# Kernel optimization log

Measured on AMD Instinct MI355X. Metric: run time of the kernel, lower is better.

The kernel has to match this reference:

```python
import jax, jax.numpy as jnp
import numpy as np

WIN = (2, 7, 7)
SHIFT = (1, 3, 3)
HEADS = 4
DIM = 128
MLP_HID = 512
N = WIN[0] * WIN[1] * WIN[2]  # 98
EPS = 1e-5


def _rel_pos_index():
    d = np.arange(WIN[0]); h = np.arange(WIN[1]); w = np.arange(WIN[2])
    coords = np.stack(np.meshgrid(d, h, w, indexing='ij'))  # (3, Wd, Wh, Ww)
    flat = coords.reshape(3, -1)  # (3, N)
    rel = flat[:, :, None] - flat[:, None, :]  # (3, N, N)
    rel = rel.transpose(1, 2, 0).astype(np.int64)  # (N, N, 3)
    rel[..., 0] += WIN[0] - 1
    rel[..., 1] += WIN[1] - 1
    rel[..., 2] += WIN[2] - 1
    rel[..., 0] *= (2 * WIN[1] - 1) * (2 * WIN[2] - 1)
    rel[..., 1] *= (2 * WIN[2] - 1)
    return rel.sum(-1)  # (N, N)


def setup_inputs() -> dict:
    key = jax.random.key(0)
    ks = jax.random.split(key, 8)
    B, D, H, W, C = 4, 8, 56, 56, DIM
    tbl_size = (2 * WIN[0] - 1) * (2 * WIN[1] - 1) * (2 * WIN[2] - 1)  # 507
    s = 0.02
    return {
        'x': jax.random.normal(ks[0], (B, D, H, W, C), jnp.float32),
        'rel_idx': jnp.asarray(_rel_pos_index(), jnp.int32),
        'rpb_table': s * jax.random.normal(ks[1], (tbl_size, HEADS), jnp.float32),
        'qkv_w': s * jax.random.normal(ks[2], (C, 3 * C), jnp.float32),
        'qkv_b': jnp.zeros((3 * C,), jnp.float32),
        'proj_w': s * jax.random.normal(ks[3], (C, C), jnp.float32),
        'proj_b': jnp.zeros((C,), jnp.float32),
        'ln1_g': jnp.ones((C,), jnp.float32),
        'ln1_b': jnp.zeros((C,), jnp.float32),
        'ln2_g': jnp.ones((C,), jnp.float32),
        'ln2_b': jnp.zeros((C,), jnp.float32),
        'mlp_w1': s * jax.random.normal(ks[4], (C, MLP_HID), jnp.float32),
        'mlp_b1': jnp.zeros((MLP_HID,), jnp.float32),
        'mlp_w2': s * jax.random.normal(ks[5], (MLP_HID, C), jnp.float32),
        'mlp_b2': jnp.zeros((C,), jnp.float32),
    }


def _layernorm(x, g, b):
    mu = jnp.mean(x, -1, keepdims=True)
    var = jnp.var(x, -1, keepdims=True)
    return (x - mu) * jax.lax.rsqrt(var + EPS) * g + b


def _window_partition(x):
    B, Dp, Hp, Wp, C = x.shape
    x = x.reshape(B, Dp // WIN[0], WIN[0], Hp // WIN[1], WIN[1], Wp // WIN[2], WIN[2], C)
    x = x.transpose(0, 1, 3, 5, 2, 4, 6, 7)
    return x.reshape(-1, N, C)


def _window_reverse(win, B, Dp, Hp, Wp):
    C = win.shape[-1]
    x = win.reshape(B, Dp // WIN[0], Hp // WIN[1], Wp // WIN[2], WIN[0], WIN[1], WIN[2], C)
    x = x.transpose(0, 1, 4, 2, 5, 3, 6, 7)
    return x.reshape(B, Dp, Hp, Wp, C)


def _block(x, rel_idx, rpb_table, qkv_w, qkv_b, proj_w, proj_b,
           ln1_g, ln1_b, ln2_g, ln2_b, mlp_w1, mlp_b1, mlp_w2, mlp_b2):
    B, D, H, W, C = x.shape
    shortcut = x
    x = _layernorm(x, ln1_g, ln1_b)
    pad_d = (-D) % WIN[0]; pad_h = (-H) % WIN[1]; pad_w = (-W) % WIN[2]
    x = jnp.pad(x, ((0, 0), (0, pad_d), (0, pad_h), (0, pad_w), (0, 0)))
    _, Dp, Hp, Wp, _ = x.shape
    x = jnp.roll(x, (-SHIFT[0], -SHIFT[1], -SHIFT[2]), axis=(1, 2, 3))
    xw = _window_partition(x)  # (B_, N, C)
    B_ = xw.shape[0]
    hd = C // HEADS
    qkv = (xw @ qkv_w + qkv_b).reshape(B_, N, 3, HEADS, hd).transpose(2, 0, 3, 1, 4)
    q, k, v = qkv[0], qkv[1], qkv[2]  # (B_, h, N, hd)
    q = q * (hd ** -0.5)
    attn = jnp.einsum('bhnd,bhmd->bhnm', q, k)
    bias = rpb_table[rel_idx.reshape(-1)].reshape(N, N, HEADS).transpose(2, 0, 1)
    attn = attn + bias[None]
    # NOTE: the original module calls attn with mask=None even when shifted.
    attn = jax.nn.softmax(attn, axis=-1)
    out = jnp.einsum('bhnm,bhmd->bhnd', attn, v).transpose(0, 2, 1, 3).reshape(B_, N, C)
    out = out @ proj_w + proj_b
    x = _window_reverse(out, B, Dp, Hp, Wp)
    x = jnp.roll(x, (SHIFT[0], SHIFT[1], SHIFT[2]), axis=(1, 2, 3))
    x = x[:, :D, :H, :W, :]
    x = shortcut + x
    h1 = _layernorm(x, ln2_g, ln2_b)
    h1 = jax.nn.gelu(h1 @ mlp_w1 + mlp_b1, approximate=False)
    return x + (h1 @ mlp_w2 + mlp_b2)


def reference(x, rel_idx, rpb_table, qkv_w, qkv_b, proj_w, proj_b,
              ln1_g, ln1_b, ln2_g, ln2_b, mlp_w1, mlp_b1, mlp_w2, mlp_b2):
    return _block(x, rel_idx, rpb_table, qkv_w, qkv_b, proj_w, proj_b,
                  ln1_g, ln1_b, ln2_g, ln2_b, mlp_w1, mlp_b1, mlp_w2, mlp_b2)
```

## Files before the change

kernel.cpp:

```cpp
#include <hip/hip_runtime.h>
#include <hip/hip_bf16.h>
#include <cstdint>

#define NWIN   1024
#define NTOK   98
#define BIAS_N 9604

typedef __attribute__((ext_vector_type(8))) short bf16x8;
typedef __attribute__((ext_vector_type(4))) float f32x4;

__device__ __forceinline__ float b2f(unsigned short u) {
  union { uint32_t i; float f; } v; v.i = ((uint32_t)u) << 16; return v.f;
}
__device__ __forceinline__ float b2f_lo(uint32_t u) {
  union { uint32_t i; float f; } v; v.i = u << 16; return v.f;
}
__device__ __forceinline__ float b2f_hi(uint32_t u) {
  union { uint32_t i; float f; } v; v.i = u & 0xffff0000u; return v.f;
}
__device__ __forceinline__ unsigned short f2b(float f) {
  union { float f; uint32_t i; } v; v.f = f;
  uint32_t r = v.i + 0x7fffu + ((v.i >> 16) & 1u);
  return (unsigned short)(r >> 16);
}
__device__ __forceinline__ float ldf(const void* p, size_t i, int f32) {
  return f32 ? ((const float*)p)[i] : b2f(((const unsigned short*)p)[i]);
}
__device__ __forceinline__ void stf(void* p, size_t i, int f32, float v) {
  if (f32) ((float*)p)[i] = v;
  else     ((unsigned short*)p)[i] = f2b(v);
}
__device__ __forceinline__ float2 ldf2(const void* p, size_t i, int f32) {
  if (f32) { const float* q = (const float*)p + i; return make_float2(q[0], q[1]); }
  uint32_t u = *(const uint32_t*)((const unsigned short*)p + i);
  return make_float2(b2f_lo(u), b2f_hi(u));
}

#define QG_OFF   0
#define KG_OFF   25690112
#define VG_OFF   51380224
#define BIAS_OFF 77070336
#define WQ_OFF   77224000
#define WP_OFF   77322304
#define W1_OFF   77355072
#define W2_OFF   77486144
#define PAR_OFF  77617216
#define FLAG_OFF 77623872
#define P_LN1G 0
#define P_LN1B 128
#define P_LN2G 256
#define P_LN2B 384
#define P_QKVB 512
#define P_PROJB 896
#define P_B1  1024
#define P_B2  1536

__global__ __launch_bounds__(256) void detect_kernel(const uint32_t* __restrict__ xw,
                                                     int* __restrict__ flag) {
  __shared__ int cnt;
  if (threadIdx.x == 0) cnt = 0;
  __syncthreads();
  uint32_t w = xw[threadIdx.x];
  int e = (w >> 23) & 0xFF;
  if (e >= 112 && e <= 134) atomicAdd(&cnt, 1);
  __syncthreads();
  if (threadIdx.x == 0) *flag = (cnt >= 128) ? 1 : 0;
}

__global__ __launch_bounds__(256) void prep_kernel(
    const void* __restrict__ qkvw, const void* __restrict__ projw,
    const void* __restrict__ w1, const void* __restrict__ w2,
    const void* __restrict__ ln1g, const void* __restrict__ ln1b,
    const void* __restrict__ ln2g, const void* __restrict__ ln2b,
    const void* __restrict__ qkvb, const void* __restrict__ projb,
    const void* __restrict__ b1, const void* __restrict__ b2,
    const int* __restrict__ flag,
    unsigned short* __restrict__ wq_t, unsigned short* __restrict__ wp_t,
    unsigned short* __restrict__ w1_t, unsigned short* __restrict__ w2_t,
    float* __restrict__ par) {
  const int f32 = *flag;
  int idx = blockIdx.x * 256 + threadIdx.x;
  if (idx < 49152) {
    int n = idx >> 7, k = idx & 127;
    wq_t[idx] = f2b(ldf(qkvw, (size_t)k * 384 + n, f32));
  } else if ((idx -= 49152) < 16384) {
    int n = idx >> 7, k = idx & 127;
    wp_t[idx] = f2b(ldf(projw, (size_t)k * 128 + n, f32));
  } else if ((idx -= 16384) < 65536) {
    int n = idx >> 7, k = idx & 127;
    w1_t[idx] = f2b(ldf(w1, (size_t)k * 512 + n, f32));
  } else if ((idx -= 65536) < 65536) {
    int n = idx >> 9, k = idx & 511;
    w2_t[idx] = f2b(ldf(w2, (size_t)k * 128 + n, f32));
  } else if ((idx -= 65536) < 1664) {
    float v;
    if      (idx < 128)  v = ldf(ln1g, idx, f32);
    else if (idx < 256)  v = ldf(ln1b, idx - 128, f32);
    else if (idx < 384)  v = ldf(ln2g, idx - 256, f32);
    else if (idx < 512)  v = ldf(ln2b, idx - 384, f32);
    else if (idx < 896)  v = ldf(qkvb, idx - 512, f32);
    else if (idx < 1024) v = ldf(projb, idx - 896, f32);
    else if (idx < 1536) v = ldf(b1, idx - 1024, f32);
    else                 v = ldf(b2, idx - 1536, f32);
    par[idx] = v;
  }
}

__global__ __launch_bounds__(256) void bias_kernel(const int* __restrict__ rel_idx,
                                                   const void* __restrict__ tbl,
                                                   const int* __restrict__ flag,
                                                   float* __restrict__ bias) {
  const int f32 = *flag;
  int i = blockIdx.x * 256 + threadIdx.x;
  if (i >= 4 * BIAS_N) return;
  int h = i / BIAS_N, ij = i % BIAS_N;
  bias[i] = ldf(tbl, (size_t)rel_idx[ij] * 4 + h, f32);
}

__global__ __launch_bounds__(256) void qkv_win_kernel(
    const void* __restrict__ x, const int* __restrict__ flag,
    const unsigned short* __restrict__ wq_t, const float* __restrict__ par,
    unsigned short* __restrict__ qg, unsigned short* __restrict__ kg,
    unsigned short* __restrict__ vg) {
  __shared__ unsigned short lnx[112 * 136];
  const int f32 = *flag;
  const int tid = threadIdx.x, wave = tid >> 6, lane = tid & 63;
  const int quad = lane >> 4, lcol = lane & 15;
  const int win = blockIdx.x;
  const int bb = win >> 8, r = win & 255;
  const int wd = r >> 6, r2 = r & 63, wh = r2 >> 3, ww = r2 & 7;

  for (int t = wave; t < NTOK; t += 4) {
    int td = t / 49, r3 = t % 49, th = r3 / 7, tw = r3 % 7;
    int sd = (wd * 2 + td + 1) & 7;
    int sh = (wh * 7 + th + 3) % 56;
    int sw = (ww * 7 + tw + 3) % 56;
    size_t src = ((((size_t)bb * 8 + sd) * 56 + sh) * 56 + sw) * 128;
    int c0 = lane * 2;
    float2 f = ldf2(x, src + c0, f32);
    float s = f.x + f.y, ss = f.x * f.x + f.y * f.y;
#pragma unroll
    for (int off = 32; off >= 1; off >>= 1) { s += __shfl_xor(s, off); ss += __shfl_xor(ss, off); }
    float mu = s * (1.0f / 128.0f);
    float var = ss * (1.0f / 128.0f) - mu * mu;
    float rs = rsqrtf(var + 1e-5f);
    float y0 = (f.x - mu) * rs * par[P_LN1G + c0] + par[P_LN1B + c0];
    float y1 = (f.y - mu) * rs * par[P_LN1G + c0 + 1] + par[P_LN1B + c0 + 1];
    *(uint32_t*)(lnx + t * 136 + c0) = (uint32_t)f2b(y0) | ((uint32_t)f2b(y1) << 16);
  }
  for (int i = tid; i < 14 * 68; i += 256) {
    int rr = i / 68, c = i % 68;
    *(uint32_t*)(lnx + (98 + rr) * 136 + c * 2) = 0u;
  }
  __syncthreads();

  for (int p = 0; p < 6; ++p) {
    const int n = p * 64 + wave * 16 + lcol;
    bf16x8 bfr[4];
#pragma unroll
    for (int ks = 0; ks < 4; ++ks)
      bfr[ks] = *(const bf16x8*)(wq_t + (size_t)n * 128 + ks * 32 + quad * 8);
    const int region = n >> 7, cc = n & 127, head = cc >> 5, d = cc & 31;
    unsigned short* dst = (region == 0 ? qg : (region == 1 ? kg : vg)) +
                          (((size_t)win * 4 + head) * NTOK) * 32 + d;
    const float bc = par[P_QKVB + n];
    const float scale = region == 0 ? 0.17677669529663687f : 1.0f;
    for (int mt = 0; mt < 7; ++mt) {
      f32x4 acc = (f32x4){0.f, 0.f, 0.f, 0.f};
#pragma unroll
      for (int ks = 0; ks < 4; ++ks) {
        bf16x8 a = *(const bf16x8*)(lnx + (mt * 16 + lcol) * 136 + ks * 32 + quad * 8);
        acc = __builtin_amdgcn_mfma_f32_16x16x32_bf16(a, bfr[ks], acc, 0, 0, 0);
      }
#pragma unroll
      for (int rr = 0; rr < 4; ++rr) {
        int m = mt * 16 + quad * 4 + rr;
        if (m < NTOK) dst[m * 32] = f2b((acc[rr] + bc) * scale);
      }
    }
  }
}

__global__ __launch_bounds__(256) void attn_fused_kernel(
    const unsigned short* __restrict__ qg, const unsigned short* __restrict__ kg,
    const unsigned short* __restrict__ vg, const float* __restrict__ bias,
    const unsigned short* __restrict__ wp_t, const float* __restrict__ par,
    const void* __restrict__ x, const int* __restrict__ flag,
    void* __restrict__ out) {
  __shared__ __align__(16) unsigned short smem[26112];
  const int f32 = *flag;
  const int tid = threadIdx.x, wave = tid >> 6, lane = tid & 63;
  const int quad = lane >> 4, lcol = lane & 15;
  const int win = blockIdx.x, h = wave;
  const size_t hb = (((size_t)win * 4 + h) * NTOK) * 32;

  unsigned short* vth = smem + h * (32 * 136);
  unsigned short* plh = smem + 17408 + h * (16 * 136);

  {
    const uint32_t* vsrc = (const uint32_t*)(vg + hb);
    for (int idx = lane; idx < NTOK * 16; idx += 64) {
      int j = idx >> 4, dp = idx & 15;
      uint32_t u = vsrc[idx];
      vth[(2 * dp) * 136 + j]     = (unsigned short)(u & 0xffffu);
      vth[(2 * dp + 1) * 136 + j] = (unsigned short)(u >> 16);
    }
    for (int idx = lane; idx < 32 * 30; idx += 64) {
      int d = idx / 30, c = 98 + idx % 30;
      vth[d * 136 + c] = 0;
    }
    for (int idx = lane; idx < 16 * 16; idx += 64) {
      int rr = idx >> 4, c = 112 + (idx & 15);
      plh[rr * 136 + c] = 0;
    }
  }

  bf16x8 aq[7], bk[7];
#pragma unroll
  for (int t = 0; t < 7; ++t) {
    int row = min(t * 16 + lcol, NTOK - 1);
    aq[t] = *(const bf16x8*)(qg + hb + (size_t)row * 32 + quad * 8);
    bk[t] = *(const bf16x8*)(kg + hb + (size_t)row * 32 + quad * 8);
  }

  const float* bh = bias + h * BIAS_N;
  f32x4 o[7][2];
  for (int mt = 0; mt < 7; ++mt) {
    f32x4 s[7];
#pragma unroll
    for (int nt = 0; nt < 7; ++nt)
      s[nt] = __builtin_amdgcn_mfma_f32_16x16x32_bf16(aq[mt], bk[nt],
                                                      (f32x4){0.f, 0.f, 0.f, 0.f}, 0, 0, 0);
    const int ib = mt * 16 + quad * 4;
#pragma unroll
    for (int nt = 0; nt < 7; ++nt) {
      int j = nt * 16 + lcol;
      bool jv = j < NTOK;
#pragma unroll
      for (int r = 0; r < 4; ++r) {
        int ic = min(ib + r, NTOK - 1);
        s[nt][r] = jv ? (s[nt][r] + bh[ic * NTOK + j]) : -3.0e38f;
      }
    }
    float mx[4], sum[4], inv[4];
#pragma unroll
    for (int r = 0; r < 4; ++r) {
      float m = s[0][r];
#pragma unroll
      for (int nt = 1; nt < 7; ++nt) m = fmaxf(m, s[nt][r]);
      mx[r] = m;
    }
#pragma unroll
    for (int off = 1; off < 16; off <<= 1)
#pragma unroll
      for (int r = 0; r < 4; ++r) mx[r] = fmaxf(mx[r], __shfl_xor(mx[r], off));
#pragma unroll
    for (int r = 0; r < 4; ++r) sum[r] = 0.f;
#pragma unroll
    for (int nt = 0; nt < 7; ++nt)
#pragma unroll
      for (int r = 0; r < 4; ++r) {
        float e = __expf(s[nt][r] - mx[r]);
        s[nt][r] = e; sum[r] += e;
      }
#pragma unroll
    for (int off = 1; off < 16; off <<= 1)
#pragma unroll
      for (int r = 0; r < 4; ++r) sum[r] += __shfl_xor(sum[r], off);
#pragma unroll
    for (int r = 0; r < 4; ++r) inv[r] = 1.0f / sum[r];
#pragma unroll
    for (int nt = 0; nt < 7; ++nt)
#pragma unroll
      for (int r = 0; r < 4; ++r)
        plh[(quad * 4 + r) * 136 + nt * 16 + lcol] = f2b(s[nt][r] * inv[r]);
#pragma unroll
    for (int n2 = 0; n2 < 2; ++n2) {
      f32x4 acc = (f32x4){0.f, 0.f, 0.f, 0.f};
#pragma unroll
      for (int kp = 0; kp < 4; ++kp) {
        bf16x8 a = *(const bf16x8*)(plh + lcol * 136 + kp * 32 + quad * 8);
        bf16x8 b = *(const bf16x8*)(vth + (n2 * 16 + lcol) * 136 + kp * 32 + quad * 8);
        acc = __builtin_amdgcn_mfma_f32_16x16x32_bf16(a, b, acc, 0, 0, 0);
      }
      o[mt][n2] = acc;
    }
  }
  __syncthreads();

  unsigned short* olds = smem;
#pragma unroll
  for (int mt = 0; mt < 7; ++mt)
#pragma unroll
    for (int n2 = 0; n2 < 2; ++n2)
#pragma unroll
      for (int r = 0; r < 4; ++r)
        olds[(mt * 16 + quad * 4 + r) * 136 + h * 32 + n2 * 16 + lcol] = f2b(o[mt][n2][r]);
  __syncthreads();

  f32x4 pr[2][7];
  for (int t2 = 0; t2 < 2; ++t2) {
    const int n = (h * 2 + t2) * 16 + lcol;
    bf16x8 bw[4];
#pragma unroll
    for (int kp = 0; kp < 4; ++kp)
      bw[kp] = *(const bf16x8*)(wp_t + (size_t)n * 128 + kp * 32 + quad * 8);
    for (int mt = 0; mt < 7; ++mt) {
      f32x4 acc = (f32x4){0.f, 0.f, 0.f, 0.f};
#pragma unroll
      for (int kp = 0; kp < 4; ++kp) {
        bf16x8 a = *(const bf16x8*)(olds + (mt * 16 + lcol) * 136 + kp * 32 + quad * 8);
        acc = __builtin_amdgcn_mfma_f32_16x16x32_bf16(a, bw[kp], acc, 0, 0, 0);
      }
      pr[t2][mt] = acc;
    }
  }
  __syncthreads();

  float* pout = (float*)smem;
  for (int t2 = 0; t2 < 2; ++t2) {
    const int n = (h * 2 + t2) * 16 + lcol;
    const float bc = par[P_PROJB + n];
#pragma unroll
    for (int mt = 0; mt < 7; ++mt)
#pragma unroll
      for (int r = 0; r < 4; ++r) {
        int m = mt * 16 + quad * 4 + r;
        if (m < NTOK) pout[m * 132 + n] = pr[t2][mt][r] + bc;
      }
  }
  __syncthreads();

  const int bb = win >> 8, rW = win & 255;
  const int wd = rW >> 6, r2 = rW & 63, wh = r2 >> 3, ww = r2 & 7;
  const int c = (tid & 31) * 4;
  for (int m = tid >> 5; m < NTOK; m += 8) {
    int td = m / 49, r3 = m % 49, th = r3 / 7, tw = r3 % 7;
    int sd = (wd * 2 + td + 1) & 7;
    int sh = (wh * 7 + th + 3) % 56;
    int sw = (ww * 7 + tw + 3) % 56;
    size_t base = ((((size_t)bb * 8 + sd) * 56 + sh) * 56 + sw) * 128 + c;
    float4 p = *(const float4*)(pout + m * 132 + c);
    if (f32) {
      const float4 xr = *(const float4*)((const float*)x + base);
      float4 ov = make_float4(p.x + xr.x, p.y + xr.y, p.z + xr.z, p.w + xr.w);
      *(float4*)((float*)out + base) = ov;
    } else {
      const ushort4 xr = *(const ushort4*)((const unsigned short*)x + base);
      ushort4 ov;
      ov.x = f2b(p.x + b2f(xr.x)); ov.y = f2b(p.y + b2f(xr.y));
      ov.z = f2b(p.z + b2f(xr.z)); ov.w = f2b(p.w + b2f(xr.w));
      *(ushort4*)((unsigned short*)out + base) = ov;
    }
  }
}

__global__ __launch_bounds__(256) void mlp_kernel(
    const unsigned short* __restrict__ w1_t, const unsigned short* __restrict__ w2_t,
    const float* __restrict__ par, const int* __restrict__ flag,
    void* __restrict__ out) {
  __shared__ __align__(16) unsigned short lnt[32 * 136];
  __shared__ __align__(16) unsigned short hbuf[32 * 264];
  const int f32 = *flag;
  const int tid = threadIdx.x, wave = tid >> 6, lane = tid & 63;
  const int quad = lane >> 4, lcol = lane & 15;
  const int m0 = blockIdx.x * 32;

  for (int t = wave; t < 32; t += 4) {
    int c0 = lane * 2;
    float2 f = ldf2(out, (size_t)(m0 + t) * 128 + c0, f32);
    float s = f.x + f.y, ss = f.x * f.x + f.y * f.y;
#pragma unroll
    for (int off = 32; off >= 1; off >>= 1) { s += __shfl_xor(s, off); ss += __shfl_xor(ss, off); }
    float mu = s * (1.0f / 128.0f);
    float var = ss * (1.0f / 128.0f) - mu * mu;
    float rs = rsqrtf(var + 1e-5f);
    float y0 = (f.x - mu) * rs * par[P_LN2G + c0] + par[P_LN2B + c0];
    float y1 = (f.y - mu) * rs * par[P_LN2G + c0 + 1] + par[P_LN2B + c0 + 1];
    *(uint32_t*)(lnt + t * 136 + c0) = (uint32_t)f2b(y0) | ((uint32_t)f2b(y1) << 16);
  }
  __syncthreads();

  f32x4 acc2[2][2];
#pragma unroll
  for (int a = 0; a < 2; ++a)
#pragma unroll
    for (int b = 0; b < 2; ++b) acc2[a][b] = (f32x4){0.f, 0.f, 0.f, 0.f};

  for (int g = 0; g < 2; ++g) {
    for (int p = 0; p < 4; ++p) {
      const int nl = p * 64 + wave * 16 + lcol;
      const int n = g * 256 + nl;
      bf16x8 bfr[4];
#pragma unroll
      for (int ks = 0; ks < 4; ++ks)
        bfr[ks] = *(const bf16x8*)(w1_t + (size_t)n * 128 + ks * 32 + quad * 8);
      const float bc = par[P_B1 + n];
#pragma unroll
      for (int mt = 0; mt < 2; ++mt) {
        f32x4 acc = (f32x4){0.f, 0.f, 0.f, 0.f};
#pragma unroll
        for (int ks = 0; ks < 4; ++ks) {
          bf16x8 a = *(const bf16x8*)(lnt + (mt * 16 + lcol) * 136 + ks * 32 + quad * 8);
          acc = __builtin_amdgcn_mfma_f32_16x16x32_bf16(a, bfr[ks], acc, 0, 0, 0);
        }
#pragma unroll
        for (int rr = 0; rr < 4; ++rr) {
          int m = mt * 16 + quad * 4 + rr;
          float v = acc[rr] + bc;
          v = 0.5f * v * (1.0f + erff(v * 0.70710678118654752f));
          hbuf[m * 264 + nl] = f2b(v);
        }
      }
    }
    __syncthreads();

#pragma unroll
    for (int np = 0; np < 2; ++np) {
      const int n = np * 64 + wave * 16 + lcol;
      for (int kp = 0; kp < 2; ++kp) {
        bf16x8 bfr[4];
#pragma unroll
        for (int ks = 0; ks < 4; ++ks)
          bfr[ks] = *(const bf16x8*)(w2_t + (size_t)n * 512 + g * 256 + kp * 128 +
                                     ks * 32 + quad * 8);
#pragma unroll
        for (int mt = 0; mt < 2; ++mt) {
#pragma unroll
          for (int ks = 0; ks < 4; ++ks) {
            bf16x8 a = *(const bf16x8*)(hbuf + (mt * 16 + lcol) * 264 + kp * 128 +
                                        ks * 32 + quad * 8);
            acc2[np][mt] = __builtin_amdgcn_mfma_f32_16x16x32_bf16(a, bfr[ks], acc2[np][mt], 0, 0, 0);
          }
        }
      }
    }
    __syncthreads();
  }

  float* pout = (float*)hbuf;
#pragma unroll
  for (int np = 0; np < 2; ++np) {
    const int n = np * 64 + wave * 16 + lcol;
    const float bc = par[P_B2 + n];
#pragma unroll
    for (int mt = 0; mt < 2; ++mt)
#pragma unroll
      for (int rr = 0; rr < 4; ++rr)
        pout[(mt * 16 + quad * 4 + rr) * 132 + n] = acc2[np][mt][rr] + bc;
  }
  __syncthreads();

  for (int i = tid; i < 1024; i += 256) {
    int t = i >> 5, c = (i & 31) * 4;
    size_t base = (size_t)(m0 + t) * 128 + c;
    float4 p = *(const float4*)(pout + t * 132 + c);
    if (f32) {
      const float4 xr = *(const float4*)((const float*)out + base);
      float4 ov = make_float4(p.x + xr.x, p.y + xr.y, p.z + xr.z, p.w + xr.w);
      *(float4*)((float*)out + base) = ov;
    } else {
      const ushort4 xr = *(const ushort4*)((const unsigned short*)out + base);
      ushort4 ov;
      ov.x = f2b(p.x + b2f(xr.x)); ov.y = f2b(p.y + b2f(xr.y));
      ov.z = f2b(p.z + b2f(xr.z)); ov.w = f2b(p.w + b2f(xr.w));
      *(ushort4*)((unsigned short*)out + base) = ov;
    }
  }
}

extern "C" void kernel_launch(void* const* d_in, const int* in_sizes, int n_in,
                              void* d_out, int out_size, void* d_ws, size_t ws_size,
                              hipStream_t stream) {
  const void* x      = d_in[0];
  const int*  rel    = (const int*)d_in[1];
  const void* rpb    = d_in[2];
  const void* qkv_w  = d_in[3];
  const void* qkv_b  = d_in[4];
  const void* proj_w = d_in[5];
  const void* proj_b = d_in[6];
  const void* ln1_g  = d_in[7];
  const void* ln1_b  = d_in[8];
  const void* ln2_g  = d_in[9];
  const void* ln2_b  = d_in[10];
  const void* w1     = d_in[11];
  const void* b1     = d_in[12];
  const void* w2     = d_in[13];
  const void* b2     = d_in[14];

  char* ws = (char*)d_ws;
  unsigned short* qg   = (unsigned short*)(ws + QG_OFF);
  unsigned short* kg   = (unsigned short*)(ws + KG_OFF);
  unsigned short* vg   = (unsigned short*)(ws + VG_OFF);
  float*          bias = (float*)(ws + BIAS_OFF);
  unsigned short* wq_t = (unsigned short*)(ws + WQ_OFF);
  unsigned short* wp_t = (unsigned short*)(ws + WP_OFF);
  unsigned short* w1_t = (unsigned short*)(ws + W1_OFF);
  unsigned short* w2_t = (unsigned short*)(ws + W2_OFF);
  float*          par  = (float*)(ws + PAR_OFF);
  int*            flag = (int*)(ws + FLAG_OFF);

  detect_kernel<<<1, 256, 0, stream>>>((const uint32_t*)x, flag);
  prep_kernel<<<775, 256, 0, stream>>>(qkv_w, proj_w, w1, w2, ln1_g, ln1_b, ln2_g,
                                       ln2_b, qkv_b, proj_b, b1, b2, flag,
                                       wq_t, wp_t, w1_t, w2_t, par);
  bias_kernel<<<(4 * BIAS_N + 255) / 256, 256, 0, stream>>>(rel, rpb, flag, bias);
  qkv_win_kernel<<<NWIN, 256, 0, stream>>>(x, flag, wq_t, par, qg, kg, vg);
  attn_fused_kernel<<<NWIN, 256, 0, stream>>>(qg, kg, vg, bias, wp_t, par, x, flag, d_out);
  mlp_kernel<<<100352 / 32, 256, 0, stream>>>(w1_t, w2_t, par, flag, d_out);
}
```

Before: 431.5 us.

## Write V pre-transposed from QKV kernel and shrink attention LDS footprint

The QKV projection kernel now writes V directly in a transposed, zero-padded (d x 112) layout to global memory, so the attention kernel reads V fragments straight from global instead of transposing V through shared memory. The attention kernel's LDS drops from about 52KB to about 30KB. The projection-output staging is split into two 56-row passes to fit the smaller buffer, and launch bounds now request 4 blocks per CU. The aim is higher occupancy and no per-block transpose, at the cost of an extra barrier pass and uncached global V loads inside the PV matmul.

```diff
diff --git a/kernel.cpp b/kernel.cpp
--- a/kernel.cpp
+++ b/kernel.cpp
@@ -38,14 +38,15 @@
 
 #define QG_OFF   0
 #define KG_OFF   25690112
-#define VG_OFF   51380224
-#define BIAS_OFF 77070336
-#define WQ_OFF   77224000
-#define WP_OFF   77322304
-#define W1_OFF   77355072
-#define W2_OFF   77486144
-#define PAR_OFF  77617216
-#define FLAG_OFF 77623872
+#define VGT_OFF  51380224
+#define ZPAD_OFF 80740352
+#define BIAS_OFF 80748544
+#define WQ_OFF   80902208
+#define WP_OFF   81000512
+#define W1_OFF   81033280
+#define W2_OFF   81164352
+#define PAR_OFF  81295424
+#define FLAG_OFF 81302080
 #define P_LN1G 0
 #define P_LN1B 128
 #define P_LN2G 256
@@ -77,7 +78,7 @@
     const int* __restrict__ flag,
     unsigned short* __restrict__ wq_t, unsigned short* __restrict__ wp_t,
     unsigned short* __restrict__ w1_t, unsigned short* __restrict__ w2_t,
-    float* __restrict__ par) {
+    float* __restrict__ par, unsigned short* __restrict__ zpad) {
   const int f32 = *flag;
   int idx = blockIdx.x * 256 + threadIdx.x;
   if (idx < 49152) {
@@ -103,6 +104,8 @@
     else if (idx < 1536) v = ldf(b1, idx - 1024, f32);
     else                 v = ldf(b2, idx - 1536, f32);
     par[idx] = v;
+  } else if ((idx -= 1664) < 4096) {
+    zpad[idx] = 0;
   }
 }
 
@@ -121,7 +124,7 @@
     const void* __restrict__ x, const int* __restrict__ flag,
     const unsigned short* __restrict__ wq_t, const float* __restrict__ par,
     unsigned short* __restrict__ qg, unsigned short* __restrict__ kg,
-    unsigned short* __restrict__ vg) {
+    unsigned short* __restrict__ vgt) {
   __shared__ unsigned short lnx[112 * 136];
   const int f32 = *flag;
   const int tid = threadIdx.x, wave = tid >> 6, lane = tid & 63;
@@ -161,58 +164,64 @@
     for (int ks = 0; ks < 4; ++ks)
       bfr[ks] = *(const bf16x8*)(wq_t + (size_t)n * 128 + ks * 32 + quad * 8);
     const int region = n >> 7, cc = n & 127, head = cc >> 5, d = cc & 31;
-    unsigned short* dst = (region == 0 ? qg : (region == 1 ? kg : vg)) +
-                          (((size_t)win * 4 + head) * NTOK) * 32 + d;
     const float bc = par[P_QKVB + n];
-    const float scale = region == 0 ? 0.17677669529663687f : 1.0f;
-    for (int mt = 0; mt < 7; ++mt) {
-      f32x4 acc = (f32x4){0.f, 0.f, 0.f, 0.f};
-#pragma unroll
-      for (int ks = 0; ks < 4; ++ks) {
-        bf16x8 a = *(const bf16x8*)(lnx + (mt * 16 + lcol) * 136 + ks * 32 + quad * 8);
-        acc = __builtin_amdgcn_mfma_f32_16x16x32_bf16(a, bfr[ks], acc, 0, 0, 0);
-      }
-#pragma unroll
-      for (int rr = 0; rr < 4; ++rr) {
-        int m = mt * 16 + quad * 4 + rr;
-        if (m < NTOK) dst[m * 32] = f2b((acc[rr] + bc) * scale);
-      }
-    }
-  }
-}
-
-__global__ __launch_bounds__(256) void attn_fused_kernel(
+    if (region < 2) {
+      unsigned short* dst = (region == 0 ? qg : kg) +
+                            (((size_t)win * 4 + head) * NTOK) * 32 + d;
+      const float scale = region == 0 ? 0.17677669529663687f : 1.0f;
+      for (int mt = 0; mt < 7; ++mt) {
+        f32x4 acc = (f32x4){0.f, 0.f, 0.f, 0.f};
+#pragma unroll
+        for (int ks = 0; ks < 4; ++ks) {
+          bf16x8 a = *(const bf16x8*)(lnx + (mt * 16 + lcol) * 136 + ks * 32 + quad * 8);
+          acc = __builtin_amdgcn_mfma_f32_16x16x32_bf16(a, bfr[ks], acc, 0, 0, 0);
+        }
+#pragma unroll
+        for (int rr = 0; rr < 4; ++rr) {
+          int m = mt * 16 + quad * 4 + rr;
+          if (m < NTOK) dst[m * 32] = f2b((acc[rr] + bc) * scale);
+        }
+      }
+    } else {
+      unsigned short* dstv = vgt + (((size_t)win * 4 + head) * 32 + d) * 112;
+      for (int mt = 0; mt < 7; ++mt) {
+        f32x4 acc = (f32x4){0.f, 0.f, 0.f, 0.f};
+#pragma unroll
+        for (int ks = 0; ks < 4; ++ks) {
+          bf16x8 a = *(const bf16x8*)(lnx + (mt * 16 + lcol) * 136 + ks * 32 + quad * 8);
+          acc = __builtin_amdgcn_mfma_f32_16x16x32_bf16(a, bfr[ks], acc, 0, 0, 0);
+        }
+        ushort4 w;
+        int m0 = mt * 16 + quad * 4;
+        w.x = (m0 + 0 < NTOK) ? f2b(acc[0] + bc) : (unsigned short)0;
+        w.y = (m0 + 1 < NTOK) ? f2b(acc[1] + bc) : (unsigned short)0;
+        w.z = (m0 + 2 < NTOK) ? f2b(acc[2] + bc) : (unsigned short)0;
+        w.w = (m0 + 3 < NTOK) ? f2b(acc[3] + bc) : (unsigned short)0;
+        *(ushort4*)(dstv + m0) = w;
+      }
+    }
+  }
+}
+
+__global__ __launch_bounds__(256, 4) void attn_fused_kernel(
     const unsigned short* __restrict__ qg, const unsigned short* __restrict__ kg,
-    const unsigned short* __restrict__ vg, const float* __restrict__ bias,
+    const unsigned short* __restrict__ vgt, const float* __restrict__ bias,
     const unsigned short* __restrict__ wp_t, const float* __restrict__ par,
     const void* __restrict__ x, const int* __restrict__ flag,
     void* __restrict__ out) {
-  __shared__ __align__(16) unsigned short smem[26112];
+  __shared__ __align__(16) unsigned short smem[15232];
   const int f32 = *flag;
   const int tid = threadIdx.x, wave = tid >> 6, lane = tid & 63;
   const int quad = lane >> 4, lcol = lane & 15;
   const int win = blockIdx.x, h = wave;
   const size_t hb = (((size_t)win * 4 + h) * NTOK) * 32;
-
-  unsigned short* vth = smem + h * (32 * 136);
-  unsigned short* plh = smem + 17408 + h * (16 * 136);
-
-  {
-    const uint32_t* vsrc = (const uint32_t*)(vg + hb);
-    for (int idx = lane; idx < NTOK * 16; idx += 64) {
-      int j = idx >> 4, dp = idx & 15;
-      uint32_t u = vsrc[idx];
-      vth[(2 * dp) * 136 + j]     = (unsigned short)(u & 0xffffu);
-      vth[(2 * dp + 1) * 136 + j] = (unsigned short)(u >> 16);
-    }
-    for (int idx = lane; idx < 32 * 30; idx += 64) {
-      int d = idx / 30, c = 98 + idx % 30;
-      vth[d * 136 + c] = 0;
-    }
-    for (int idx = lane; idx < 16 * 16; idx += 64) {
-      int rr = idx >> 4, c = 112 + (idx & 15);
-      plh[rr * 136 + c] = 0;
-    }
+  const unsigned short* vbase = vgt + (((size_t)win * 4 + h) * 32) * 112;
+
+  unsigned short* plh = smem + h * (16 * 132);
+
+  for (int idx = lane; idx < 16 * 16; idx += 64) {
+    int rr = idx >> 4, c = 112 + (idx & 15);
+    plh[rr * 132 + c] = 0;
   }
 
   bf16x8 aq[7], bk[7];
@@ -273,14 +282,15 @@
     for (int nt = 0; nt < 7; ++nt)
 #pragma unroll
       for (int r = 0; r < 4; ++r)
-        plh[(quad * 4 + r) * 136 + nt * 16 + lcol] = f2b(s[nt][r] * inv[r]);
+        plh[(quad * 4 + r) * 132 + nt * 16 + lcol] = f2b(s[nt][r] * inv[r]);
 #pragma unroll
     for (int n2 = 0; n2 < 2; ++n2) {
       f32x4 acc = (f32x4){0.f, 0.f, 0.f, 0.f};
 #pragma unroll
       for (int kp = 0; kp < 4; ++kp) {
-        bf16x8 a = *(const bf16x8*)(plh + lcol * 136 + kp * 32 + quad * 8);
-        bf16x8 b = *(const bf16x8*)(vth + (n2 * 16 + lcol) * 136 + kp * 32 + quad * 8);
+        bf16x8 a = *(const bf16x8*)(plh + lcol * 132 + kp * 32 + quad * 8);
+        bf16x8 b = *(const bf16x8*)(vbase + (size_t)(n2 * 16 + lcol) * 112 +
+                                    kp * 32 + quad * 8);
         acc = __builtin_amdgcn_mfma_f32_16x16x32_bf16(a, b, acc, 0, 0, 0);
       }
       o[mt][n2] = acc;
@@ -317,41 +327,47 @@
   }
   __syncthreads();
 
-  float* pout = (float*)smem;
-  for (int t2 = 0; t2 < 2; ++t2) {
-    const int n = (h * 2 + t2) * 16 + lcol;
-    const float bc = par[P_PROJB + n];
-#pragma unroll
-    for (int mt = 0; mt < 7; ++mt)
-#pragma unroll
-      for (int r = 0; r < 4; ++r) {
-        int m = mt * 16 + quad * 4 + r;
-        if (m < NTOK) pout[m * 132 + n] = pr[t2][mt][r] + bc;
-      }
-  }
-  __syncthreads();
-
   const int bb = win >> 8, rW = win & 255;
   const int wd = rW >> 6, r2 = rW & 63, wh = r2 >> 3, ww = r2 & 7;
-  const int c = (tid & 31) * 4;
-  for (int m = tid >> 5; m < NTOK; m += 8) {
-    int td = m / 49, r3 = m % 49, th = r3 / 7, tw = r3 % 7;
-    int sd = (wd * 2 + td + 1) & 7;
-    int sh = (wh * 7 + th + 3) % 56;
-    int sw = (ww * 7 + tw + 3) % 56;
-    size_t base = ((((size_t)bb * 8 + sd) * 56 + sh) * 56 + sw) * 128 + c;
-    float4 p = *(const float4*)(pout + m * 132 + c);
-    if (f32) {
-      const float4 xr = *(const float4*)((const float*)x + base);
-      float4 ov = make_float4(p.x + xr.x, p.y + xr.y, p.z + xr.z, p.w + xr.w);
-      *(float4*)((float*)out + base) = ov;
-    } else {
-      const ushort4 xr = *(const ushort4*)((const unsigned short*)x + base);
-      ushort4 ov;
-      ov.x = f2b(p.x + b2f(xr.x)); ov.y = f2b(p.y + b2f(xr.y));
-      ov.z = f2b(p.z + b2f(xr.z)); ov.w = f2b(p.w + b2f(xr.w));
-      *(ushort4*)((unsigned short*)out + base) = ov;
-    }
+  float* pout = (float*)smem;
+  for (int pass = 0; pass < 2; ++pass) {
+    const int mlo = pass * 56;
+    for (int t2 = 0; t2 < 2; ++t2) {
+      const int n = (h * 2 + t2) * 16 + lcol;
+      const float bc = par[P_PROJB + n];
+#pragma unroll
+      for (int mt = 0; mt < 7; ++mt)
+#pragma unroll
+        for (int r = 0; r < 4; ++r) {
+          int m = mt * 16 + quad * 4 + r;
+          if (m >= mlo && m < mlo + 56 && m < NTOK)
+            pout[(m - mlo) * 132 + n] = pr[t2][mt][r] + bc;
+        }
+    }
+    __syncthreads();
+    const int c = (tid & 31) * 4;
+    for (int i = tid >> 5; i < 56; i += 8) {
+      int m = mlo + i;
+      if (m >= NTOK) break;
+      int td = m / 49, r3 = m % 49, th = r3 / 7, tw = r3 % 7;
+      int sd = (wd * 2 + td + 1) & 7;
+      int sh = (wh * 7 + th + 3) % 56;
+      int sw = (ww * 7 + tw + 3) % 56;
+      size_t base = ((((size_t)bb * 8 + sd) * 56 + sh) * 56 + sw) * 128 + c;
+      float4 p = *(const float4*)(pout + i * 132 + c);
+      if (f32) {
+        const float4 xr = *(const float4*)((const float*)x + base);
+        float4 ov = make_float4(p.x + xr.x, p.y + xr.y, p.z + xr.z, p.w + xr.w);
+        *(float4*)((float*)out + base) = ov;
+      } else {
+        const ushort4 xr = *(const ushort4*)((const unsigned short*)x + base);
+        ushort4 ov;
+        ov.x = f2b(p.x + b2f(xr.x)); ov.y = f2b(p.y + b2f(xr.y));
+        ov.z = f2b(p.z + b2f(xr.z)); ov.w = f2b(p.w + b2f(xr.w));
+        *(ushort4*)((unsigned short*)out + base) = ov;
+      }
+    }
+    if (pass == 0) __syncthreads();
   }
 }
 
@@ -491,7 +507,8 @@
   char* ws = (char*)d_ws;
   unsigned short* qg   = (unsigned short*)(ws + QG_OFF);
   unsigned short* kg   = (unsigned short*)(ws + KG_OFF);
-  unsigned short* vg   = (unsigned short*)(ws + VG_OFF);
+  unsigned short* vgt  = (unsigned short*)(ws + VGT_OFF);
+  unsigned short* zpad = (unsigned short*)(ws + ZPAD_OFF);
   float*          bias = (float*)(ws + BIAS_OFF);
   unsigned short* wq_t = (unsigned short*)(ws + WQ_OFF);
   unsigned short* wp_t = (unsigned short*)(ws + WP_OFF);
@@ -501,11 +518,11 @@
   int*            flag = (int*)(ws + FLAG_OFF);
 
   detect_kernel<<<1, 256, 0, stream>>>((const uint32_t*)x, flag);
-  prep_kernel<<<775, 256, 0, stream>>>(qkv_w, proj_w, w1, w2, ln1_g, ln1_b, ln2_g,
+  prep_kernel<<<791, 256, 0, stream>>>(qkv_w, proj_w, w1, w2, ln1_g, ln1_b, ln2_g,
                                        ln2_b, qkv_b, proj_b, b1, b2, flag,
-                                       wq_t, wp_t, w1_t, w2_t, par);
+                                       wq_t, wp_t, w1_t, w2_t, par, zpad);
   bias_kernel<<<(4 * BIAS_N + 255) / 256, 256, 0, stream>>>(rel, rpb, flag, bias);
-  qkv_win_kernel<<<NWIN, 256, 0, stream>>>(x, flag, wq_t, par, qg, kg, vg);
-  attn_fused_kernel<<<NWIN, 256, 0, stream>>>(qg, kg, vg, bias, wp_t, par, x, flag, d_out);
+  qkv_win_kernel<<<NWIN, 256, 0, stream>>>(x, flag, wq_t, par, qg, kg, vgt);
+  attn_fused_kernel<<<NWIN, 256, 0, stream>>>(qg, kg, vgt, bias, wp_t, par, x, flag, d_out);
   mlp_kernel<<<100352 / 32, 256, 0, stream>>>(w1_t, w2_t, par, flag, d_out);
 }
```

New measurement: 404.1 us. -6.4%, faster.
